# Kernel tuning notes

Measured on AMD Instinct MI355X. Metric: run time of the kernel, lower is better.

## Reference

```python
import jax, jax.numpy as jnp
import numpy as np

N, D, K = 65536, 64, 64


def setup_inputs() -> dict:
    key = jax.random.key(0)
    k1, k2, k3, k4, k5 = jax.random.split(key, 5)
    # seed z = (u, x): u ~ U[0,1), x ~ N(0, I_d)
    u = jax.random.uniform(k1, (N, 1), dtype=jnp.float32)
    x = jax.random.normal(k2, (N, D), dtype=jnp.float32)
    z = jnp.concatenate([u, x], axis=-1)  # [N, d+1]
    # parameters, sized/initialized as in GaussianMixture.__init__
    means = 3.0 * jax.random.normal(k3, (K, D), dtype=jnp.float32)
    devsqrt = jnp.eye(D, dtype=jnp.float32) + 0.3 * jax.random.normal(k4, (K, D, D), dtype=jnp.float32)
    devs = jnp.einsum('kij,klj->kil', devsqrt, devsqrt)  # devsqrt @ devsqrt.T per mode
    mix = jax.nn.softmax(jax.random.normal(k5, (K,), dtype=jnp.float32))
    mix_partition = jnp.cumsum(mix)  # [K], monotone boundaries in (0, 1]
    return {"z": z, "means": means, "devs": devs, "mix_partition": mix_partition}


def reference(z, means, devs, mix_partition):
    # split z -> (u, x)
    u = z[..., 0]          # [N]
    x = z[..., 1:]         # [N, d]
    k = means.shape[0]
    # torch.bucketize(u, partition, right=True) == searchsorted side='right'
    idx = jnp.searchsorted(mix_partition, u, side='right')
    idx = jnp.clip(idx, 0, k - 1)  # guard u == 1.0 edge case
    # y = means[i] + devs[i] @ x  (gather fused with batched matvec)
    dy = jnp.einsum('nij,nj->ni', devs[idx], x)
    return means[idx] + dy
```

## Files before the change

### kernel.cpp

```cpp
#include <hip/hip_runtime.h>
#include <hip/hip_bf16.h>
#include <stdint.h>

#define NROWS 65536
#define KMIX 64
#define DD 64
#define ZS 65
#define CHUNK 128
#define PADN (NROWS + KMIX * CHUNK)
#define NBLK4 (PADN / CHUNK)

typedef __bf16 bf16x8 __attribute__((ext_vector_type(8)));
typedef float f32x4 __attribute__((ext_vector_type(4)));

__device__ __forceinline__ unsigned short f2bf(float f) {
  unsigned int x = __float_as_uint(f);
  unsigned int r = (x + 0x7FFFu + ((x >> 16) & 1u)) >> 16;
  return (unsigned short)r;
}

__global__ __launch_bounds__(256) void k_idx(
    const float* __restrict__ z, const float* __restrict__ mix,
    uint32_t* __restrict__ idx_arr, uint32_t* __restrict__ bh) {
  __shared__ float s_mix[KMIX];
  __shared__ uint32_t s_hist[KMIX];
  int t = threadIdx.x;
  if (t < KMIX) { s_mix[t] = mix[t]; s_hist[t] = 0u; }
  __syncthreads();
  int n = blockIdx.x * 256 + t;
  float u = z[n * ZS];
  int idx = 0;
  #pragma unroll
  for (int k = 0; k < KMIX; ++k) idx += (s_mix[k] <= u) ? 1 : 0;
  if (idx > KMIX - 1) idx = KMIX - 1;
  idx_arr[n] = (uint32_t)idx;
  atomicAdd(&s_hist[idx], 1u);
  __syncthreads();
  if (t < KMIX) bh[blockIdx.x * KMIX + t] = s_hist[t];
}

__global__ void k_scan(const uint32_t* __restrict__ bh,
                       uint32_t* __restrict__ counts,
                       uint32_t* __restrict__ offsets,
                       uint32_t* __restrict__ cursors) {
  __shared__ uint32_t s_c[KMIX];
  int t = threadIdx.x;
  uint32_t c = 0;
  for (int b = 0; b < NROWS / 256; ++b) c += bh[b * KMIX + t];
  s_c[t] = c;
  counts[t] = c;
  __syncthreads();
  if (t == 0) {
    uint32_t off = 0;
    for (int k = 0; k < KMIX; ++k) {
      offsets[k] = off;
      cursors[k] = off;
      off += ((s_c[k] + CHUNK - 1) / CHUNK) * CHUNK;
    }
    offsets[KMIX] = off;
  }
}

__global__ __launch_bounds__(256) void k_scatter(
    const uint32_t* __restrict__ idx_arr,
    uint32_t* __restrict__ cursors, uint32_t* __restrict__ sorted) {
  __shared__ uint32_t h[KMIX];
  __shared__ uint32_t base[KMIX];
  int t = threadIdx.x;
  if (t < KMIX) h[t] = 0u;
  __syncthreads();
  int n = blockIdx.x * 256 + t;
  uint32_t k = idx_arr[n];
  uint32_t r = atomicAdd(&h[k], 1u);
  __syncthreads();
  if (t < KMIX) base[t] = h[t] ? atomicAdd(&cursors[t], h[t]) : 0u;
  __syncthreads();
  sorted[base[k] + r] = (uint32_t)n;
}

__global__ __launch_bounds__(256) void k_main(
    const float* __restrict__ z, const float* __restrict__ means,
    const float* __restrict__ devs, const uint32_t* __restrict__ sorted,
    const uint32_t* __restrict__ counts, const uint32_t* __restrict__ offsets,
    float* __restrict__ out) {
  __shared__ uint32_t s_ent[CHUNK];
  __shared__ __align__(16) unsigned short s_devs[DD * 72];
  __shared__ __align__(16) unsigned short s_x[CHUNK * 72];

  const int t = threadIdx.x;
  const int base = blockIdx.x * CHUNK;

  int kb = 0;
  while (kb < KMIX - 1 && offsets[kb + 1] <= (uint32_t)base) ++kb;
  int nv = (int)counts[kb] - (base - (int)offsets[kb]);
  if (nv <= 0) return;
  if (nv > CHUNK) nv = CHUNK;

  if (t < CHUNK) s_ent[t] = (t < nv) ? sorted[base + t] : 0u;
  __syncthreads();

  {
    const float4* gd = reinterpret_cast<const float4*>(devs + (size_t)kb * DD * DD);
    #pragma unroll
    for (int it = 0; it < 4; ++it) {
      int e = t + it * 256;
      float4 v = gd[e];
      int row = e >> 4, col = (e & 15) * 4;
      ushort4 w = make_ushort4(f2bf(v.x), f2bf(v.y), f2bf(v.z), f2bf(v.w));
      *reinterpret_cast<ushort4*>(&s_devs[row * 72 + col]) = w;
    }
  }
  {
    int lane = t & 63, wr = t >> 6;
    #pragma unroll
    for (int rr = 0; rr < CHUNK; rr += 4) {
      int rl = rr + wr;
      uint32_t row = s_ent[rl];
      float xv = z[(size_t)row * ZS + 1 + lane];
      s_x[rl * 72 + lane] = f2bf(xv);
    }
  }
  __syncthreads();

  const int lane = t & 63, wave = t >> 6;
  const int m16 = lane & 15, quad = lane >> 4;

  float mv[4];
  #pragma unroll
  for (int it = 0; it < 4; ++it) mv[it] = means[kb * DD + it * 16 + m16];

  for (int g = wave; g < CHUNK / 16; g += 4) {
    const unsigned short* xr = &s_x[(g * 16 + m16) * 72 + quad * 8];
    bf16x8 a0 = *reinterpret_cast<const bf16x8*>(xr);
    bf16x8 a1 = *reinterpret_cast<const bf16x8*>(xr + 32);

    f32x4 acc[4];
    #pragma unroll
    for (int it = 0; it < 4; ++it) acc[it] = (f32x4){0.f, 0.f, 0.f, 0.f};

    #pragma unroll
    for (int it = 0; it < 4; ++it) {
      const unsigned short* dr = &s_devs[(it * 16 + m16) * 72 + quad * 8];
      bf16x8 b0 = *reinterpret_cast<const bf16x8*>(dr);
      bf16x8 b1 = *reinterpret_cast<const bf16x8*>(dr + 32);
      acc[it] = __builtin_amdgcn_mfma_f32_16x16x32_bf16(a0, b0, acc[it], 0, 0, 0);
      acc[it] = __builtin_amdgcn_mfma_f32_16x16x32_bf16(a1, b1, acc[it], 0, 0, 0);
    }

    #pragma unroll
    for (int reg = 0; reg < 4; ++reg) {
      int rp = g * 16 + quad * 4 + reg;
      if (rp < nv) {
        uint32_t row = s_ent[rp];
        float* orow = out + (size_t)row * DD + m16;
        #pragma unroll
        for (int it = 0; it < 4; ++it) orow[it * 16] = acc[it][reg] + mv[it];
      }
    }
  }
}

extern "C" void kernel_launch(void* const* d_in, const int* in_sizes, int n_in,
                              void* d_out, int out_size, void* d_ws, size_t ws_size,
                              hipStream_t stream) {
  const float* z     = (const float*)d_in[0];
  const float* means = (const float*)d_in[1];
  const float* devs  = (const float*)d_in[2];
  const float* mix   = (const float*)d_in[3];
  float* out = (float*)d_out;

  uint32_t* W = (uint32_t*)d_ws;
  uint32_t* idx_arr = W;
  uint32_t* bh      = idx_arr + NROWS;
  uint32_t* counts  = bh + (NROWS / 256) * KMIX;
  uint32_t* offsets = counts + KMIX;
  uint32_t* cursors = offsets + KMIX + 1;
  uint32_t* sorted  = cursors + KMIX;

  k_idx<<<NROWS / 256, 256, 0, stream>>>(z, mix, idx_arr, bh);
  k_scan<<<1, KMIX, 0, stream>>>(bh, counts, offsets, cursors);
  k_scatter<<<NROWS / 256, 256, 0, stream>>>(idx_arr, cursors, sorted);
  k_main<<<NBLK4, 256, 0, stream>>>(z, means, devs, sorted, counts, offsets, out);
}
```

Before: 95.47 us.

## Replace single-block scan kernel with global atomics and per-block wave scans

Drops the serial one-block k_scan kernel. Per-block histograms are now accumulated with global atomics into counts, and each block of the scatter and main kernels recomputes the padded prefix offsets with a wave-level shuffle scan. This removes one launch and a serial loop over 256 block histograms, at the cost of an added memset and some redundant scan work in every block. Cursors now start from zero and have the offset added locally.

```diff
diff --git a/kernel.cpp b/kernel.cpp
--- a/kernel.cpp
+++ b/kernel.cpp
@@ -19,9 +19,23 @@
   return (unsigned short)r;
 }
 
+__device__ __forceinline__ void scan_offsets(const uint32_t* __restrict__ counts,
+                                             uint32_t* __restrict__ s_off, int t) {
+  uint32_t c = counts[t];
+  uint32_t p = ((c + CHUNK - 1) / CHUNK) * CHUNK;
+  uint32_t inc = p;
+  #pragma unroll
+  for (int d = 1; d < 64; d <<= 1) {
+    uint32_t v = __shfl_up(inc, d, 64);
+    if (t >= d) inc += v;
+  }
+  s_off[t] = inc - p;
+  if (t == 63) s_off[64] = inc;
+}
+
 __global__ __launch_bounds__(256) void k_idx(
     const float* __restrict__ z, const float* __restrict__ mix,
-    uint32_t* __restrict__ idx_arr, uint32_t* __restrict__ bh) {
+    uint32_t* __restrict__ idx_arr, uint32_t* __restrict__ counts) {
   __shared__ float s_mix[KMIX];
   __shared__ uint32_t s_hist[KMIX];
   int t = threadIdx.x;
@@ -36,44 +50,23 @@
   idx_arr[n] = (uint32_t)idx;
   atomicAdd(&s_hist[idx], 1u);
   __syncthreads();
-  if (t < KMIX) bh[blockIdx.x * KMIX + t] = s_hist[t];
-}
-
-__global__ void k_scan(const uint32_t* __restrict__ bh,
-                       uint32_t* __restrict__ counts,
-                       uint32_t* __restrict__ offsets,
-                       uint32_t* __restrict__ cursors) {
-  __shared__ uint32_t s_c[KMIX];
-  int t = threadIdx.x;
-  uint32_t c = 0;
-  for (int b = 0; b < NROWS / 256; ++b) c += bh[b * KMIX + t];
-  s_c[t] = c;
-  counts[t] = c;
-  __syncthreads();
-  if (t == 0) {
-    uint32_t off = 0;
-    for (int k = 0; k < KMIX; ++k) {
-      offsets[k] = off;
-      cursors[k] = off;
-      off += ((s_c[k] + CHUNK - 1) / CHUNK) * CHUNK;
-    }
-    offsets[KMIX] = off;
-  }
+  if (t < KMIX && s_hist[t]) atomicAdd(&counts[t], s_hist[t]);
 }
 
 __global__ __launch_bounds__(256) void k_scatter(
-    const uint32_t* __restrict__ idx_arr,
+    const uint32_t* __restrict__ idx_arr, const uint32_t* __restrict__ counts,
     uint32_t* __restrict__ cursors, uint32_t* __restrict__ sorted) {
+  __shared__ uint32_t s_off[KMIX + 1];
   __shared__ uint32_t h[KMIX];
   __shared__ uint32_t base[KMIX];
   int t = threadIdx.x;
-  if (t < KMIX) h[t] = 0u;
+  if (t < KMIX) { h[t] = 0u; scan_offsets(counts, s_off, t); }
   __syncthreads();
   int n = blockIdx.x * 256 + t;
   uint32_t k = idx_arr[n];
   uint32_t r = atomicAdd(&h[k], 1u);
   __syncthreads();
-  if (t < KMIX) base[t] = h[t] ? atomicAdd(&cursors[t], h[t]) : 0u;
+  if (t < KMIX) base[t] = s_off[t] + (h[t] ? atomicAdd(&cursors[t], h[t]) : 0u);
   __syncthreads();
   sorted[base[k] + r] = (uint32_t)n;
 }
@@ -81,8 +74,8 @@
 __global__ __launch_bounds__(256) void k_main(
     const float* __restrict__ z, const float* __restrict__ means,
     const float* __restrict__ devs, const uint32_t* __restrict__ sorted,
-    const uint32_t* __restrict__ counts, const uint32_t* __restrict__ offsets,
-    float* __restrict__ out) {
+    const uint32_t* __restrict__ counts, float* __restrict__ out) {
+  __shared__ uint32_t s_off[KMIX + 1];
   __shared__ uint32_t s_ent[CHUNK];
   __shared__ __align__(16) unsigned short s_devs[DD * 72];
   __shared__ __align__(16) unsigned short s_x[CHUNK * 72];
@@ -90,9 +83,12 @@
   const int t = threadIdx.x;
   const int base = blockIdx.x * CHUNK;
 
+  if (t < KMIX) scan_offsets(counts, s_off, t);
+  __syncthreads();
+
   int kb = 0;
-  while (kb < KMIX - 1 && offsets[kb + 1] <= (uint32_t)base) ++kb;
-  int nv = (int)counts[kb] - (base - (int)offsets[kb]);
+  while (kb < KMIX - 1 && s_off[kb + 1] <= (uint32_t)base) ++kb;
+  int nv = (int)counts[kb] - (base - (int)s_off[kb]);
   if (nv <= 0) return;
   if (nv > CHUNK) nv = CHUNK;
 
@@ -170,15 +166,14 @@
   float* out = (float*)d_out;
 
   uint32_t* W = (uint32_t*)d_ws;
-  uint32_t* idx_arr = W;
-  uint32_t* bh      = idx_arr + NROWS;
-  uint32_t* counts  = bh + (NROWS / 256) * KMIX;
-  uint32_t* offsets = counts + KMIX;
-  uint32_t* cursors = offsets + KMIX + 1;
-  uint32_t* sorted  = cursors + KMIX;
+  uint32_t* counts  = W;
+  uint32_t* cursors = counts + KMIX;
+  uint32_t* idx_arr = cursors + KMIX;
+  uint32_t* sorted  = idx_arr + NROWS;
 
-  k_idx<<<NROWS / 256, 256, 0, stream>>>(z, mix, idx_arr, bh);
-  k_scan<<<1, KMIX, 0, stream>>>(bh, counts, offsets, cursors);
-  k_scatter<<<NROWS / 256, 256, 0, stream>>>(idx_arr, cursors, sorted);
-  k_main<<<NBLK4, 256, 0, stream>>>(z, means, devs, sorted, counts, offsets, out);
+  hipMemsetAsync(W, 0, 2 * KMIX * sizeof(uint32_t), stream);
+
+  k_idx<<<NROWS / 256, 256, 0, stream>>>(z, mix, idx_arr, counts);
+  k_scatter<<<NROWS / 256, 256, 0, stream>>>(idx_arr, counts, cursors, sorted);
+  k_main<<<NBLK4, 256, 0, stream>>>(z, means, devs, sorted, counts, out);
 }
```

Result: no change. 94.80 us (-0.7%).
